# Optimization experiments

Measured on AMD Instinct MI355X. Metric: run time of the kernel, lower is better.

Reference implementation:

```python
import jax, jax.numpy as jnp
import numpy as np

N = 20000      # tuple-graph nodes
E = 320000     # edges per relation
F_IN = 5189    # 80 one-hot + 3*1703 node features
DIM = 256
N_ORIG = 183   # original texas graph nodes
C = 7


def _gcn(x, W, b, src, dst, n):
    # PyG GCNConv: add self loops, symmetric deg^-1/2 normalization, aggregate src->dst.
    loop = jnp.arange(n)
    s = jnp.concatenate([src, loop])
    d = jnp.concatenate([dst, loop])
    deg = jax.ops.segment_sum(jnp.ones(s.shape[0], x.dtype), d, num_segments=n)
    dinv = jnp.where(deg > 0, jax.lax.rsqrt(deg), 0.0)
    norm = dinv[s] * dinv[d]            # [E+n]
    h = x @ W                            # [n, dim]
    out = jax.ops.segment_sum(h[s] * norm[:, None], d, num_segments=n)
    return out + b


def _mlp(h, w1, b1, w2, b2):
    return jnp.maximum(h @ w1 + b1, 0.0) @ w2 + b2


def _seg_mean(h, idx, n):
    s = jax.ops.segment_sum(h, idx, num_segments=n)
    cnt = jax.ops.segment_sum(jnp.ones(idx.shape[0], h.dtype), idx, num_segments=n)
    return s / jnp.maximum(cnt, 1.0)[:, None]


def setup_inputs() -> dict:
    key = jax.random.key(0)
    ks = jax.random.split(key, 16)
    sc_in = 1.0 / np.sqrt(F_IN)
    sc_d = 1.0 / np.sqrt(DIM)
    sc_3d = 1.0 / np.sqrt(3 * DIM)
    inp = {
        'x': jax.random.normal(ks[0], (N, F_IN), jnp.float32),
        'w1': jax.random.normal(ks[1], (3, F_IN, DIM), jnp.float32) * sc_in,
        'b1': jnp.zeros((3, DIM), jnp.float32),
        'w2': jax.random.normal(ks[2], (3, DIM, DIM), jnp.float32) * sc_d,
        'b2': jnp.zeros((3, DIM), jnp.float32),
        'm1w1': jax.random.normal(ks[3], (3 * DIM, DIM), jnp.float32) * sc_3d,
        'm1b1': jnp.zeros((DIM,), jnp.float32),
        'm1w2': jax.random.normal(ks[4], (DIM, DIM), jnp.float32) * sc_d,
        'm1b2': jnp.zeros((DIM,), jnp.float32),
        'm2w1': jax.random.normal(ks[5], (3 * DIM, DIM), jnp.float32) * sc_3d,
        'm2b1': jnp.zeros((DIM,), jnp.float32),
        'm2w2': jax.random.normal(ks[6], (DIM, DIM), jnp.float32) * sc_d,
        'm2b2': jnp.zeros((DIM,), jnp.float32),
        'mw1': jax.random.normal(ks[7], (3 * DIM, DIM), jnp.float32) * sc_3d,
        'mb1': jnp.zeros((DIM,), jnp.float32),
        'mw2': jax.random.normal(ks[8], (DIM, C), jnp.float32) * sc_d,
        'mb2': jnp.zeros((C,), jnp.float32),
        'edge_index_1': jax.random.randint(ks[9], (2, E), 0, N),
        'edge_index_2': jax.random.randint(ks[10], (2, E), 0, N),
        'edge_index_3': jax.random.randint(ks[11], (2, E), 0, N),
        'index_1': jax.random.randint(ks[12], (N,), 0, N_ORIG),
        'index_2': jax.random.randint(ks[13], (N,), 0, N_ORIG),
        'index_3': jax.random.randint(ks[14], (N,), 0, N_ORIG),
    }
    return inp


def reference(x, w1, b1, w2, b2, m1w1, m1b1, m1w2, m1b2,
              m2w1, m2b1, m2w2, m2b2, mw1, mb1, mw2, mb2,
              edge_index_1, edge_index_2, edge_index_3,
              index_1, index_2, index_3):
    n = x.shape[0]
    eis = (edge_index_1, edge_index_2, edge_index_3)
    # layer 1: three GCN convs over the three relations, ReLU, concat, MLP
    hs = [jnp.maximum(_gcn(x, w1[i], b1[i], eis[i][0], eis[i][1], n), 0.0) for i in range(3)]
    h = _mlp(jnp.concatenate(hs, axis=-1), m1w1, m1b1, m1w2, m1b2)
    # layer 2
    hs = [jnp.maximum(_gcn(h, w2[i], b2[i], eis[i][0], eis[i][1], n), 0.0) for i in range(3)]
    h = _mlp(jnp.concatenate(hs, axis=-1), m2w1, m2b1, m2w2, m2b2)
    # faithful to source bug: index_2 is overwritten by index_3 before scatter
    x1 = _seg_mean(h, index_1, N_ORIG)
    x2 = _seg_mean(h, index_3, N_ORIG)
    x3 = _seg_mean(h, index_3, N_ORIG)
    out = _mlp(jnp.concatenate([x1, x2, x3], axis=1), mw1, mb1, mw2, mb2)
    return jax.nn.log_softmax(out, axis=1)
```

## Files before the change

kernel.cpp:

```cpp
#include <hip/hip_runtime.h>
#include <hip/hip_bf16.h>
#include <cstdint>
#include <cstddef>

typedef __bf16 bf16_t;
typedef __bf16 bf16x8 __attribute__((ext_vector_type(8)));
typedef __bf16 bf16x4 __attribute__((ext_vector_type(4)));
typedef float f32x4 __attribute__((ext_vector_type(4)));

#define NN 20000
#define NE 320000
#define FIN 5189
#define KP1 5216
#define NORIG 183

__device__ inline f32x4 ld4u(const float* p) {
  f32x4 v; __builtin_memcpy(&v, p, 16); return v;
}

__device__ inline void gload_lds16(const bf16_t* g, bf16_t* l) {
  __builtin_amdgcn_global_load_lds(
      (const __attribute__((address_space(1))) uint32_t*)g,
      (__attribute__((address_space(3))) uint32_t*)l, 16, 0, 0);
}

__device__ inline int swz(int r) { return (r ^ (r >> 2)) & 3; }

__global__ void k_cvtpad(const float* __restrict__ x, bf16_t* __restrict__ xb) {
  const int total = NN * (KP1 / 8);
  for (int idx = blockIdx.x * 256 + threadIdx.x; idx < total; idx += gridDim.x * 256) {
    int row = idx / (KP1 / 8);
    int c8  = idx - row * (KP1 / 8);
    int col = c8 * 8;
    bf16x8 v{};
    const float* xp = x + (size_t)row * FIN + col;
    if (col + 8 <= FIN) {
      f32x4 a = ld4u(xp), b = ld4u(xp + 4);
#pragma unroll
      for (int j = 0; j < 4; ++j) { v[j] = (bf16_t)a[j]; v[4 + j] = (bf16_t)b[j]; }
    } else {
#pragma unroll
      for (int j = 0; j < 8; ++j) v[j] = (col + j < FIN) ? (bf16_t)xp[j] : (bf16_t)0.f;
    }
    *(bf16x8*)&xb[(size_t)row * KP1 + col] = v;
  }
}

__global__ __launch_bounds__(512) void k_gemm_w(
    const bf16_t* __restrict__ A, const bf16_t* __restrict__ Bt,
    bf16_t* __restrict__ C, const float* __restrict__ bias,
    int M, int N, int Kp, int relu)
{
  __shared__ __align__(16) bf16_t As[2][128 * 32];
  __shared__ __align__(16) bf16_t Bs[2][256 * 32];
  const int tid = threadIdx.x, lane = tid & 63, wave = tid >> 6;
  const int m0 = blockIdx.y * 128, n0 = blockIdx.x * 256;
  const int wr = (wave >> 2) * 64, wc = (wave & 3) * 64;
  const int fm = lane & 15, fs = lane >> 4;

  const int arow = tid >> 2, asl = tid & 3;
  const int aks = asl ^ swz(arow);
  int agrow = m0 + arow; if (agrow >= M) agrow = M - 1;
  const bf16_t* asrc = A + (size_t)agrow * Kp + aks * 8;

  const int br0 = tid >> 2, br1 = 128 + br0;
  const bf16_t* bsrc0 = Bt + (size_t)(n0 + br0) * Kp + (asl ^ swz(br0)) * 8;
  const bf16_t* bsrc1 = Bt + (size_t)(n0 + br1) * Kp + (asl ^ swz(br1)) * 8;

  bf16_t* adst  = &As[0][0] + wave * 512;
  bf16_t* bdst0 = &Bs[0][0] + wave * 512;
  bf16_t* bdst1 = &Bs[0][0] + 4096 + wave * 512;

  int aoff[4], boff[4];
#pragma unroll
  for (int i = 0; i < 4; ++i) {
    int ra = wr + i * 16 + fm;
    aoff[i] = ra * 32 + (fs ^ swz(ra)) * 8;
    int rb = wc + i * 16 + fm;
    boff[i] = rb * 32 + (fs ^ swz(rb)) * 8;
  }

  f32x4 acc[4][4];
#pragma unroll
  for (int i = 0; i < 4; ++i)
#pragma unroll
    for (int j = 0; j < 4; ++j) acc[i][j] = {0.f, 0.f, 0.f, 0.f};

#define STAGEW(buf, kof) do { \
    gload_lds16(asrc + (kof),  adst  + (buf) * (128 * 32)); \
    gload_lds16(bsrc0 + (kof), bdst0 + (buf) * (256 * 32)); \
    gload_lds16(bsrc1 + (kof), bdst1 + (buf) * (256 * 32)); \
  } while (0)

  const int NT = Kp / 32;
  STAGEW(0, 0);
  __syncthreads();
  int buf = 0;
  for (int t = 0; t < NT - 1; ++t) {
    STAGEW(buf ^ 1, (t + 1) * 32);
    bf16x8 af[4], bfv[4];
#pragma unroll
    for (int i = 0; i < 4; ++i) af[i] = *(const bf16x8*)&As[buf][aoff[i]];
#pragma unroll
    for (int j = 0; j < 4; ++j) bfv[j] = *(const bf16x8*)&Bs[buf][boff[j]];
#pragma unroll
    for (int i = 0; i < 4; ++i)
#pragma unroll
      for (int j = 0; j < 4; ++j)
        acc[i][j] = __builtin_amdgcn_mfma_f32_16x16x32_bf16(af[i], bfv[j], acc[i][j], 0, 0, 0);
    __syncthreads();
    buf ^= 1;
  }
  {
    bf16x8 af[4], bfv[4];
#pragma unroll
    for (int i = 0; i < 4; ++i) af[i] = *(const bf16x8*)&As[buf][aoff[i]];
#pragma unroll
    for (int j = 0; j < 4; ++j) bfv[j] = *(const bf16x8*)&Bs[buf][boff[j]];
#pragma unroll
    for (int i = 0; i < 4; ++i)
#pragma unroll
      for (int j = 0; j < 4; ++j)
        acc[i][j] = __builtin_amdgcn_mfma_f32_16x16x32_bf16(af[i], bfv[j], acc[i][j], 0, 0, 0);
  }

  const int ccol = n0 + wc + fm;
#pragma unroll
  for (int i = 0; i < 4; ++i) {
    const int rb2 = m0 + wr + i * 16 + (lane >> 4) * 4;
#pragma unroll
    for (int r = 0; r < 4; ++r) {
      const int row = rb2 + r;
      if (row < M) {
        bf16_t* cp = C + (size_t)row * N + ccol;
#pragma unroll
        for (int j = 0; j < 4; ++j) {
          float v = acc[i][j][r];
          if (bias) v += bias[ccol + j * 16];
          if (relu) v = fmaxf(v, 0.f);
          cp[j * 16] = (bf16_t)v;
        }
      }
    }
  }
}

__global__ __launch_bounds__(256) void k_gemm_s(
    const bf16_t* __restrict__ A, const bf16_t* __restrict__ Bt,
    bf16_t* __restrict__ C, const float* __restrict__ bias,
    int M, int N, int Kp, int relu)
{
  __shared__ __align__(16) bf16_t As[2][128 * 32];
  __shared__ __align__(16) bf16_t Bs[2][128 * 32];
  const int tid = threadIdx.x, lane = tid & 63, wave = tid >> 6;
  const int m0 = blockIdx.y * 128, n0 = blockIdx.x * 128;
  const int wr = (wave >> 1) * 64, wc = (wave & 1) * 64;
  const int fm = lane & 15, fs = lane >> 4;

  const int r0 = tid >> 2, r1 = 64 + r0, sl = tid & 3;
  int ag0 = m0 + r0; if (ag0 >= M) ag0 = M - 1;
  int ag1 = m0 + r1; if (ag1 >= M) ag1 = M - 1;
  const bf16_t* asrc0 = A + (size_t)ag0 * Kp + (sl ^ swz(r0)) * 8;
  const bf16_t* asrc1 = A + (size_t)ag1 * Kp + (sl ^ swz(r1)) * 8;
  const bf16_t* bsrc0 = Bt + (size_t)(n0 + r0) * Kp + (sl ^ swz(r0)) * 8;
  const bf16_t* bsrc1 = Bt + (size_t)(n0 + r1) * Kp + (sl ^ swz(r1)) * 8;

  bf16_t* adst0 = &As[0][0] + wave * 512;
  bf16_t* adst1 = &As[0][0] + 2048 + wave * 512;
  bf16_t* bdst0 = &Bs[0][0] + wave * 512;
  bf16_t* bdst1 = &Bs[0][0] + 2048 + wave * 512;

  int aoff[4], boff[4];
#pragma unroll
  for (int i = 0; i < 4; ++i) {
    int ra = wr + i * 16 + fm;
    aoff[i] = ra * 32 + (fs ^ swz(ra)) * 8;
    int rb = wc + i * 16 + fm;
    boff[i] = rb * 32 + (fs ^ swz(rb)) * 8;
  }

  f32x4 acc[4][4];
#pragma unroll
  for (int i = 0; i < 4; ++i)
#pragma unroll
    for (int j = 0; j < 4; ++j) acc[i][j] = {0.f, 0.f, 0.f, 0.f};

#define STAGES(buf, kof) do { \
    gload_lds16(asrc0 + (kof), adst0 + (buf) * (128 * 32)); \
    gload_lds16(asrc1 + (kof), adst1 + (buf) * (128 * 32)); \
    gload_lds16(bsrc0 + (kof), bdst0 + (buf) * (128 * 32)); \
    gload_lds16(bsrc1 + (kof), bdst1 + (buf) * (128 * 32)); \
  } while (0)

  const int NT = Kp / 32;
  STAGES(0, 0);
  __syncthreads();
  int buf = 0;
  for (int t = 0; t < NT - 1; ++t) {
    STAGES(buf ^ 1, (t + 1) * 32);
    bf16x8 af[4], bfv[4];
#pragma unroll
    for (int i = 0; i < 4; ++i) af[i] = *(const bf16x8*)&As[buf][aoff[i]];
#pragma unroll
    for (int j = 0; j < 4; ++j) bfv[j] = *(const bf16x8*)&Bs[buf][boff[j]];
#pragma unroll
    for (int i = 0; i < 4; ++i)
#pragma unroll
      for (int j = 0; j < 4; ++j)
        acc[i][j] = __builtin_amdgcn_mfma_f32_16x16x32_bf16(af[i], bfv[j], acc[i][j], 0, 0, 0);
    __syncthreads();
    buf ^= 1;
  }
  {
    bf16x8 af[4], bfv[4];
#pragma unroll
    for (int i = 0; i < 4; ++i) af[i] = *(const bf16x8*)&As[buf][aoff[i]];
#pragma unroll
    for (int j = 0; j < 4; ++j) bfv[j] = *(const bf16x8*)&Bs[buf][boff[j]];
#pragma unroll
    for (int i = 0; i < 4; ++i)
#pragma unroll
      for (int j = 0; j < 4; ++j)
        acc[i][j] = __builtin_amdgcn_mfma_f32_16x16x32_bf16(af[i], bfv[j], acc[i][j], 0, 0, 0);
  }

  const int ccol = n0 + wc + fm;
#pragma unroll
  for (int i = 0; i < 4; ++i) {
    const int rb2 = m0 + wr + i * 16 + (lane >> 4) * 4;
#pragma unroll
    for (int r = 0; r < 4; ++r) {
      const int row = rb2 + r;
      if (row < M) {
        bf16_t* cp = C + (size_t)row * N + ccol;
#pragma unroll
        for (int j = 0; j < 4; ++j) {
          float v = acc[i][j][r];
          if (bias) v += bias[ccol + j * 16];
          if (relu) v = fmaxf(v, 0.f);
          cp[j * 16] = (bf16_t)v;
        }
      }
    }
  }
}

__global__ void k_transw(const float* __restrict__ src, bf16_t* __restrict__ dst,
                         int K, int Kp)
{
  __shared__ float tile[32][33];
  const int g = blockIdx.z;
  const int k0 = blockIdx.x * 32, j0 = blockIdx.y * 32;
  const int tx = threadIdx.x, ty = threadIdx.y;
  const float* sp = src + (size_t)g * K * 256;
#pragma unroll
  for (int i = 0; i < 4; ++i) {
    int k = k0 + ty + i * 8;
    tile[ty + i * 8][tx] = (k < K) ? sp[(size_t)k * 256 + j0 + tx] : 0.f;
  }
  __syncthreads();
  bf16_t* dp = dst + (size_t)g * 256 * Kp;
#pragma unroll
  for (int i = 0; i < 4; ++i) {
    int n = j0 + ty + i * 8;
    dp[(size_t)n * Kp + k0 + tx] = (bf16_t)tile[tx][ty + i * 8];
  }
}

__global__ void k_deg(const int* __restrict__ dst, int* __restrict__ cnt, int E) {
  int e = blockIdx.x * 256 + threadIdx.x;
  if (e < E) atomicAdd(&cnt[dst[e]], 1);
}

__global__ void k_dinv(const int* __restrict__ deg, float* __restrict__ dinv) {
  int v = blockIdx.x * 256 + threadIdx.x;
  if (v < 3 * NN) dinv[v] = rsqrtf((float)(deg[v] + 1));
}

#define SCAN_T 1024
#define SCAN_CH 20
__global__ __launch_bounds__(SCAN_T) void k_scan(
    const int* __restrict__ deg, int* __restrict__ rp, int* __restrict__ cur)
{
  const int r = blockIdx.x;
  const int* d = deg + r * NN;
  int* rpr = rp + r * (NN + 1);
  int* cr  = cur + r * NN;
  __shared__ int ts[SCAN_T];
  const int t = threadIdx.x;
  const int base = t * SCAN_CH;
  int local[SCAN_CH];
  int sum = 0;
#pragma unroll
  for (int i = 0; i < SCAN_CH; ++i) {
    int v = base + i;
    int x = (v < NN) ? d[v] : 0;
    local[i] = sum; sum += x;
  }
  ts[t] = sum; __syncthreads();
  for (int ofs = 1; ofs < SCAN_T; ofs <<= 1) {
    int v = ts[t];
    int w = (t >= ofs) ? ts[t - ofs] : 0;
    __syncthreads();
    ts[t] = v + w;
    __syncthreads();
  }
  int excl = (t == 0) ? 0 : ts[t - 1];
#pragma unroll
  for (int i = 0; i < SCAN_CH; ++i) {
    int v = base + i;
    if (v < NN) { int val = excl + local[i]; rpr[v] = val; cr[v] = val; }
  }
  if (t == SCAN_T - 1) rpr[NN] = ts[SCAN_T - 1];
}

__global__ void k_bucket(const int* __restrict__ src, const int* __restrict__ dst,
                         int* __restrict__ cur, int* __restrict__ col) {
  int e = blockIdx.x * 256 + threadIdx.x;
  if (e < NE) {
    int d = dst[e];
    int pos = atomicAdd(&cur[d], 1);
    col[pos] = src[e];
  }
}

__global__ __launch_bounds__(256) void k_gatherb(
    const bf16_t* __restrict__ H, bf16_t* __restrict__ Out,
    const int* __restrict__ rp, const int* __restrict__ col,
    const float* __restrict__ dinv, const float* __restrict__ bias)
{
  const int wv = threadIdx.x >> 6, lane = threadIdx.x & 63;
  const int v = blockIdx.x * 4 + wv;
  const int r = blockIdx.y;
  const int roff = r << 8;
  const int* rpr = rp + r * (NN + 1);
  const int* cr  = col + (size_t)r * NE;
  const float* dvp = dinv + r * NN;
  const float dv = dvp[v];
  const int c0 = roff + lane * 4;

  bf16x4 hs = *(const bf16x4*)&H[(size_t)v * 768 + c0];
  float a0 = (float)hs[0] * dv, a1 = (float)hs[1] * dv,
        a2 = (float)hs[2] * dv, a3 = (float)hs[3] * dv;

  int i = rpr[v];
  const int e = rpr[v + 1];
  for (; i + 2 <= e; i += 2) {
    int s0 = cr[i], s1 = cr[i + 1];
    float d0 = dvp[s0], d1 = dvp[s1];
    bf16x4 h0 = *(const bf16x4*)&H[(size_t)s0 * 768 + c0];
    bf16x4 h1 = *(const bf16x4*)&H[(size_t)s1 * 768 + c0];
    a0 += (float)h0[0] * d0 + (float)h1[0] * d1;
    a1 += (float)h0[1] * d0 + (float)h1[1] * d1;
    a2 += (float)h0[2] * d0 + (float)h1[2] * d1;
    a3 += (float)h0[3] * d0 + (float)h1[3] * d1;
  }
  if (i < e) {
    int s = cr[i];
    float d = dvp[s];
    bf16x4 h = *(const bf16x4*)&H[(size_t)s * 768 + c0];
    a0 += (float)h[0] * d; a1 += (float)h[1] * d;
    a2 += (float)h[2] * d; a3 += (float)h[3] * d;
  }
  f32x4 bb = ld4u(bias + c0);
  bf16x4 o;
  o[0] = (bf16_t)fmaxf(dv * a0 + bb[0], 0.f);
  o[1] = (bf16_t)fmaxf(dv * a1 + bb[1], 0.f);
  o[2] = (bf16_t)fmaxf(dv * a2 + bb[2], 0.f);
  o[3] = (bf16_t)fmaxf(dv * a3 + bb[3], 0.f);
  *(bf16x4*)&Out[(size_t)v * 768 + c0] = o;
}

__global__ void k_segscatter(const bf16_t* __restrict__ h2,
                             const int* __restrict__ i1, const int* __restrict__ i3,
                             float* __restrict__ s1, float* __restrict__ s3,
                             float* __restrict__ c1, float* __restrict__ c3) {
  int v = blockIdx.x, c = threadIdx.x;
  float val = (float)h2[(size_t)v * 256 + c];
  int g1 = i1[v], g3 = i3[v];
  atomicAdd(&s1[g1 * 256 + c], val);
  atomicAdd(&s3[g3 * 256 + c], val);
  if (c == 0) { atomicAdd(&c1[g1], 1.f); atomicAdd(&c3[g3], 1.f); }
}

__global__ __launch_bounds__(256) void k_final(
    const float* __restrict__ s1, const float* __restrict__ s3,
    const float* __restrict__ c1, const float* __restrict__ c3,
    const float* __restrict__ mw1, const float* __restrict__ mb1,
    const float* __restrict__ mw2, const float* __restrict__ mb2,
    float* __restrict__ out)
{
  __shared__ float xc[768];
  __shared__ float tt[256];
  __shared__ float lg[8];
  const int g = blockIdx.x, tid = threadIdx.x;
  float inv1 = 1.f / fmaxf(c1[g], 1.f);
  float inv3 = 1.f / fmaxf(c3[g], 1.f);
  float a3 = s3[g * 256 + tid] * inv3;
  xc[tid] = s1[g * 256 + tid] * inv1;
  xc[256 + tid] = a3;
  xc[512 + tid] = a3;
  __syncthreads();
  float acc = mb1[tid];
  for (int k = 0; k < 768; ++k) acc += xc[k] * mw1[k * 256 + tid];
  tt[tid] = fmaxf(acc, 0.f);
  __syncthreads();
  if (tid < 7) {
    float a = mb2[tid];
    for (int k = 0; k < 256; ++k) a += tt[k] * mw2[k * 7 + tid];
    lg[tid] = a;
  }
  __syncthreads();
  if (tid == 0) {
    float mx = lg[0];
    for (int c2 = 1; c2 < 7; ++c2) mx = fmaxf(mx, lg[c2]);
    float sum = 0.f;
    for (int c2 = 0; c2 < 7; ++c2) sum += expf(lg[c2] - mx);
    float lse = logf(sum) + mx;
    for (int c2 = 0; c2 < 7; ++c2) out[g * 7 + c2] = lg[c2] - lse;
  }
}

extern "C" void kernel_launch(void* const* d_in, const int* in_sizes, int n_in,
                              void* d_out, int out_size, void* d_ws, size_t ws_size,
                              hipStream_t stream) {
  const float* x    = (const float*)d_in[0];
  const float* w1   = (const float*)d_in[1];
  const float* b1   = (const float*)d_in[2];
  const float* w2   = (const float*)d_in[3];
  const float* b2   = (const float*)d_in[4];
  const float* m1w1 = (const float*)d_in[5];
  const float* m1b1 = (const float*)d_in[6];
  const float* m1w2 = (const float*)d_in[7];
  const float* m1b2 = (const float*)d_in[8];
  const float* m2w1 = (const float*)d_in[9];
  const float* m2b1 = (const float*)d_in[10];
  const float* m2w2 = (const float*)d_in[11];
  const float* m2b2 = (const float*)d_in[12];
  const float* mw1  = (const float*)d_in[13];
  const float* mb1  = (const float*)d_in[14];
  const float* mw2  = (const float*)d_in[15];
  const float* mb2  = (const float*)d_in[16];
  const int* e1 = (const int*)d_in[17];
  const int* e2 = (const int*)d_in[18];
  const int* e3 = (const int*)d_in[19];
  const int* i1 = (const int*)d_in[20];
  const int* i3 = (const int*)d_in[22];
  float* out = (float*)d_out;

  char* ws = (char*)d_ws;
  size_t off = 0;
  auto alloc = [&](size_t bytes) {
    char* p = ws + off;
    off += (bytes + 255) & ~(size_t)255;
    return (void*)p;
  };
  bf16_t* xb   = (bf16_t*)alloc((size_t)NN * KP1 * 2);
  bf16_t* wt   = (bf16_t*)alloc((size_t)768 * KP1 * 2);
  bf16_t* a1   = (bf16_t*)alloc((size_t)NN * 768 * 2);
  bf16_t* g1   = (bf16_t*)alloc((size_t)NN * 768 * 2);
  bf16_t* t1   = (bf16_t*)alloc((size_t)NN * 256 * 2);
  bf16_t* h1   = (bf16_t*)alloc((size_t)NN * 256 * 2);
  int*    deg  = (int*)alloc((size_t)3 * NN * 4);
  float*  dinv = (float*)alloc((size_t)3 * NN * 4);
  int*    rp   = (int*)alloc((size_t)3 * (NN + 1) * 4);
  int*    cur  = (int*)alloc((size_t)3 * NN * 4);
  int*    col  = (int*)alloc((size_t)3 * NE * 4);
  float*  s1   = (float*)alloc((size_t)NORIG * 256 * 4);
  float*  s3   = (float*)alloc((size_t)NORIG * 256 * 4);
  float*  c1   = (float*)alloc((size_t)NORIG * 4);
  float*  c3   = (float*)alloc((size_t)NORIG * 4);

  hipMemsetAsync(deg, 0, (size_t)3 * NN * 4, stream);
  int gb = (NE + 255) / 256;
  k_deg<<<gb, 256, 0, stream>>>(e1 + NE, deg + 0 * NN, NE);
  k_deg<<<gb, 256, 0, stream>>>(e2 + NE, deg + 1 * NN, NE);
  k_deg<<<gb, 256, 0, stream>>>(e3 + NE, deg + 2 * NN, NE);
  k_dinv<<<(3 * NN + 255) / 256, 256, 0, stream>>>(deg, dinv);
  k_scan<<<3, SCAN_T, 0, stream>>>(deg, rp, cur);
  k_bucket<<<gb, 256, 0, stream>>>(e1, e1 + NE, cur + 0 * NN, col + 0 * (size_t)NE);
  k_bucket<<<gb, 256, 0, stream>>>(e2, e2 + NE, cur + 1 * NN, col + 1 * (size_t)NE);
  k_bucket<<<gb, 256, 0, stream>>>(e3, e3 + NE, cur + 2 * NN, col + 2 * (size_t)NE);

  auto transw = [&](const float* Wsrc, int G, int K, int Kp) {
    k_transw<<<dim3(Kp / 32, 8, G), dim3(32, 8), 0, stream>>>(Wsrc, wt, K, Kp);
  };

  dim3 ggat(NN / 4, 3);

  transw(w1, 3, FIN, KP1);
  k_cvtpad<<<2048, 256, 0, stream>>>(x, xb);
  k_gemm_w<<<dim3(3, 157), 512, 0, stream>>>(xb, wt, a1, nullptr, NN, 768, KP1, 0);
  k_gatherb<<<ggat, 256, 0, stream>>>(a1, g1, rp, col, dinv, b1);
  transw(m1w1, 1, 768, 768);
  k_gemm_s<<<dim3(2, 157), 256, 0, stream>>>(g1, wt, t1, m1b1, NN, 256, 768, 1);
  transw(m1w2, 1, 256, 256);
  k_gemm_s<<<dim3(2, 157), 256, 0, stream>>>(t1, wt, h1, m1b2, NN, 256, 256, 0);

  transw(w2, 3, 256, 256);
  k_gemm_w<<<dim3(3, 157), 512, 0, stream>>>(h1, wt, a1, nullptr, NN, 768, 256, 0);
  k_gatherb<<<ggat, 256, 0, stream>>>(a1, g1, rp, col, dinv, b2);
  transw(m2w1, 1, 768, 768);
  k_gemm_s<<<dim3(2, 157), 256, 0, stream>>>(g1, wt, t1, m2b1, NN, 256, 768, 1);
  transw(m2w2, 1, 256, 256);
  k_gemm_s<<<dim3(2, 157), 256, 0, stream>>>(t1, wt, h1, m2b2, NN, 256, 256, 0);

  hipMemsetAsync(s1, 0, (size_t)NORIG * 256 * 4, stream);
  hipMemsetAsync(s3, 0, (size_t)NORIG * 256 * 4, stream);
  hipMemsetAsync(c1, 0, (size_t)NORIG * 4, stream);
  hipMemsetAsync(c3, 0, (size_t)NORIG * 4, stream);
  k_segscatter<<<NN, 256, 0, stream>>>(h1, i1, i3, s1, s3, c1, c3);
  k_final<<<NORIG, 256, 0, stream>>>(s1, s3, c1, c3, mw1, mb1, mw2, mb2, out);
}
```

Measured before the change: 898.9 us.

## Enlarge wide GEMM tile to 256x256 with 4-stage global-to-LDS pipeline

Replaces the 128x256 double-buffered wide GEMM with a 256x256 tile per block, each wave computing 128x64, and a four-buffer ring that prefetches three K-steps ahead using explicit vmcnt waits and raw barriers. It also raises MFMA priority during the compute section. The aim is more operand reuse per LDS load and hiding of global-load latency in the large feature GEMM. The cost is 128 KB of LDS and many more accumulator registers, which limit occupancy, and a grid of 237 blocks that may underfill the CUs.

```diff
diff --git a/kernel.cpp b/kernel.cpp
--- a/kernel.cpp
+++ b/kernel.cpp
@@ -46,87 +46,93 @@
   }
 }
 
-__global__ __launch_bounds__(512) void k_gemm_w(
+__global__ __launch_bounds__(512, 2) void k_gemm8(
     const bf16_t* __restrict__ A, const bf16_t* __restrict__ Bt,
     bf16_t* __restrict__ C, const float* __restrict__ bias,
     int M, int N, int Kp, int relu)
 {
-  __shared__ __align__(16) bf16_t As[2][128 * 32];
-  __shared__ __align__(16) bf16_t Bs[2][256 * 32];
+  __shared__ __align__(16) bf16_t As[4][256 * 32];
+  __shared__ __align__(16) bf16_t Bs[4][256 * 32];
   const int tid = threadIdx.x, lane = tid & 63, wave = tid >> 6;
-  const int m0 = blockIdx.y * 128, n0 = blockIdx.x * 256;
-  const int wr = (wave >> 2) * 64, wc = (wave & 3) * 64;
+  const int m0 = blockIdx.y * 256, n0 = blockIdx.x * 256;
+  const int wr = (wave >> 2) * 128, wc = (wave & 3) * 64;
   const int fm = lane & 15, fs = lane >> 4;
 
-  const int arow = tid >> 2, asl = tid & 3;
-  const int aks = asl ^ swz(arow);
-  int agrow = m0 + arow; if (agrow >= M) agrow = M - 1;
-  const bf16_t* asrc = A + (size_t)agrow * Kp + aks * 8;
-
-  const int br0 = tid >> 2, br1 = 128 + br0;
-  const bf16_t* bsrc0 = Bt + (size_t)(n0 + br0) * Kp + (asl ^ swz(br0)) * 8;
-  const bf16_t* bsrc1 = Bt + (size_t)(n0 + br1) * Kp + (asl ^ swz(br1)) * 8;
-
-  bf16_t* adst  = &As[0][0] + wave * 512;
-  bf16_t* bdst0 = &Bs[0][0] + wave * 512;
-  bf16_t* bdst1 = &Bs[0][0] + 4096 + wave * 512;
-
-  int aoff[4], boff[4];
-#pragma unroll
-  for (int i = 0; i < 4; ++i) {
+  const int rA0 = 32 * wave + (lane >> 2);
+  const int rA1 = rA0 + 16;
+  const int p0 = lane & 3;
+  int gmA0 = m0 + rA0; if (gmA0 >= M) gmA0 = M - 1;
+  int gmA1 = m0 + rA1; if (gmA1 >= M) gmA1 = M - 1;
+  const bf16_t* srcA0 = A + (size_t)gmA0 * Kp + (p0 ^ swz(rA0)) * 8;
+  const bf16_t* srcA1 = A + (size_t)gmA1 * Kp + (p0 ^ swz(rA1)) * 8;
+  const bf16_t* srcB0 = Bt + (size_t)(n0 + rA0) * Kp + (p0 ^ swz(rA0)) * 8;
+  const bf16_t* srcB1 = Bt + (size_t)(n0 + rA1) * Kp + (p0 ^ swz(rA1)) * 8;
+  const int dst0 = 1024 * wave;
+  const int dst1 = 1024 * wave + 512;
+
+  int aoff[8], boff[4];
+#pragma unroll
+  for (int i = 0; i < 8; ++i) {
     int ra = wr + i * 16 + fm;
     aoff[i] = ra * 32 + (fs ^ swz(ra)) * 8;
-    int rb = wc + i * 16 + fm;
-    boff[i] = rb * 32 + (fs ^ swz(rb)) * 8;
-  }
-
-  f32x4 acc[4][4];
-#pragma unroll
-  for (int i = 0; i < 4; ++i)
+  }
+#pragma unroll
+  for (int j = 0; j < 4; ++j) {
+    int rb = wc + j * 16 + fm;
+    boff[j] = rb * 32 + (fs ^ swz(rb)) * 8;
+  }
+
+  f32x4 acc[8][4];
+#pragma unroll
+  for (int i = 0; i < 8; ++i)
 #pragma unroll
     for (int j = 0; j < 4; ++j) acc[i][j] = {0.f, 0.f, 0.f, 0.f};
 
-#define STAGEW(buf, kof) do { \
-    gload_lds16(asrc + (kof),  adst  + (buf) * (128 * 32)); \
-    gload_lds16(bsrc0 + (kof), bdst0 + (buf) * (256 * 32)); \
-    gload_lds16(bsrc1 + (kof), bdst1 + (buf) * (256 * 32)); \
+#define STG8(s) do { \
+    const int b_ = (s) & 3; const int ko_ = (s) * 32; \
+    gload_lds16(srcA0 + ko_, &As[b_][0] + dst0); \
+    gload_lds16(srcA1 + ko_, &As[b_][0] + dst1); \
+    gload_lds16(srcB0 + ko_, &Bs[b_][0] + dst0); \
+    gload_lds16(srcB1 + ko_, &Bs[b_][0] + dst1); \
   } while (0)
 
   const int NT = Kp / 32;
-  STAGEW(0, 0);
-  __syncthreads();
-  int buf = 0;
-  for (int t = 0; t < NT - 1; ++t) {
-    STAGEW(buf ^ 1, (t + 1) * 32);
-    bf16x8 af[4], bfv[4];
-#pragma unroll
-    for (int i = 0; i < 4; ++i) af[i] = *(const bf16x8*)&As[buf][aoff[i]];
-#pragma unroll
-    for (int j = 0; j < 4; ++j) bfv[j] = *(const bf16x8*)&Bs[buf][boff[j]];
-#pragma unroll
-    for (int i = 0; i < 4; ++i)
+  STG8(0); STG8(1); STG8(2);
+  __builtin_amdgcn_sched_barrier(0);
+  asm volatile("s_waitcnt vmcnt(8)" ::: "memory");
+  __builtin_amdgcn_s_barrier();
+  __builtin_amdgcn_sched_barrier(0);
+
+  for (int t = 0; t < NT; ++t) {
+    const int nxt = t + 3;
+    if (nxt < NT) STG8(nxt);
+    const int b = t & 3;
+    bf16x8 af[8], bfv[4];
+#pragma unroll
+    for (int j = 0; j < 4; ++j) bfv[j] = *(const bf16x8*)&Bs[b][boff[j]];
+#pragma unroll
+    for (int i = 0; i < 8; ++i) af[i] = *(const bf16x8*)&As[b][aoff[i]];
+    __builtin_amdgcn_s_setprio(1);
+#pragma unroll
+    for (int i = 0; i < 8; ++i)
 #pragma unroll
       for (int j = 0; j < 4; ++j)
         acc[i][j] = __builtin_amdgcn_mfma_f32_16x16x32_bf16(af[i], bfv[j], acc[i][j], 0, 0, 0);
-    __syncthreads();
-    buf ^= 1;
-  }
-  {
-    bf16x8 af[4], bfv[4];
-#pragma unroll
-    for (int i = 0; i < 4; ++i) af[i] = *(const bf16x8*)&As[buf][aoff[i]];
-#pragma unroll
-    for (int j = 0; j < 4; ++j) bfv[j] = *(const bf16x8*)&Bs[buf][boff[j]];
-#pragma unroll
-    for (int i = 0; i < 4; ++i)
-#pragma unroll
-      for (int j = 0; j < 4; ++j)
-        acc[i][j] = __builtin_amdgcn_mfma_f32_16x16x32_bf16(af[i], bfv[j], acc[i][j], 0, 0, 0);
-  }
+    __builtin_amdgcn_s_setprio(0);
+    if (t < NT - 1) {
+      __builtin_amdgcn_sched_barrier(0);
+      if (nxt < NT)            asm volatile("s_waitcnt vmcnt(8) lgkmcnt(0)" ::: "memory");
+      else if (nxt == NT)      asm volatile("s_waitcnt vmcnt(4) lgkmcnt(0)" ::: "memory");
+      else                     asm volatile("s_waitcnt vmcnt(0) lgkmcnt(0)" ::: "memory");
+      __builtin_amdgcn_s_barrier();
+      __builtin_amdgcn_sched_barrier(0);
+    }
+  }
+#undef STG8
 
   const int ccol = n0 + wc + fm;
 #pragma unroll
-  for (int i = 0; i < 4; ++i) {
+  for (int i = 0; i < 8; ++i) {
     const int rb2 = m0 + wr + i * 16 + (lane >> 4) * 4;
 #pragma unroll
     for (int r = 0; r < 4; ++r) {
@@ -490,7 +496,7 @@
 
   transw(w1, 3, FIN, KP1);
   k_cvtpad<<<2048, 256, 0, stream>>>(x, xb);
-  k_gemm_w<<<dim3(3, 157), 512, 0, stream>>>(xb, wt, a1, nullptr, NN, 768, KP1, 0);
+  k_gemm8<<<dim3(3, 79), 512, 0, stream>>>(xb, wt, a1, nullptr, NN, 768, KP1, 0);
   k_gatherb<<<ggat, 256, 0, stream>>>(a1, g1, rp, col, dinv, b1);
   transw(m1w1, 1, 768, 768);
   k_gemm_s<<<dim3(2, 157), 256, 0, stream>>>(g1, wt, t1, m1b1, NN, 256, 768, 1);
@@ -498,7 +504,7 @@
   k_gemm_s<<<dim3(2, 157), 256, 0, stream>>>(t1, wt, h1, m1b2, NN, 256, 256, 0);
 
   transw(w2, 3, 256, 256);
-  k_gemm_w<<<dim3(3, 157), 512, 0, stream>>>(h1, wt, a1, nullptr, NN, 768, 256, 0);
+  k_gemm8<<<dim3(3, 79), 512, 0, stream>>>(h1, wt, a1, nullptr, NN, 768, 256, 0);
   k_gatherb<<<ggat, 256, 0, stream>>>(a1, g1, rp, col, dinv, b2);
   transw(m2w1, 1, 768, 768);
   k_gemm_s<<<dim3(2, 157), 256, 0, stream>>>(g1, wt, t1, m2b1, NN, 256, 768, 1);
```

Result: slower. 961.3 us (+6.9%).

## Replace atomic segment-mean with CSR gather, merge degree/bucket kernels, XCD-remap GEMM

Applied to the files above, without the earlier changes.

The float-atomic scatter used for the final segment means is replaced by a CSR build over the 183 groups (count, scan, bucket) and a gather-based reduction inside the final MLP kernel. The per-relation degree and bucket kernels are merged into single launches. The wide GEMM now uses a 1D grid with a chiplet-aware (XCD) block remap for better L2 locality, and the edge-gather loop is unrolled by four. This removes about 10M float atomics and several launches and memsets, but the final kernel now serially reads about 110 rows per group per thread.

```diff
diff --git a/kernel.cpp b/kernel.cpp
--- a/kernel.cpp
+++ b/kernel.cpp
@@ -49,12 +49,18 @@
 __global__ __launch_bounds__(512) void k_gemm_w(
     const bf16_t* __restrict__ A, const bf16_t* __restrict__ Bt,
     bf16_t* __restrict__ C, const float* __restrict__ bias,
-    int M, int N, int Kp, int relu)
+    int M, int N, int Kp, int relu, int NBX)
 {
   __shared__ __align__(16) bf16_t As[2][128 * 32];
   __shared__ __align__(16) bf16_t Bs[2][256 * 32];
+  const int nwg = gridDim.x;
+  const int q = nwg >> 3, rr = nwg & 7;
+  const int xcd = blockIdx.x & 7, jj = blockIdx.x >> 3;
+  const int L = (xcd < rr ? xcd * (q + 1) : rr * (q + 1) + (xcd - rr) * q) + jj;
+  const int bx = L % NBX, by = L / NBX;
+
   const int tid = threadIdx.x, lane = tid & 63, wave = tid >> 6;
-  const int m0 = blockIdx.y * 128, n0 = blockIdx.x * 256;
+  const int m0 = by * 128, n0 = bx * 256;
   const int wr = (wave >> 2) * 64, wc = (wave & 3) * 64;
   const int fm = lane & 15, fs = lane >> 4;
 
@@ -267,9 +273,22 @@
   }
 }
 
-__global__ void k_deg(const int* __restrict__ dst, int* __restrict__ cnt, int E) {
-  int e = blockIdx.x * 256 + threadIdx.x;
-  if (e < E) atomicAdd(&cnt[dst[e]], 1);
+__global__ void k_deg3(const int* __restrict__ e1, const int* __restrict__ e2,
+                       const int* __restrict__ e3, int* __restrict__ deg) {
+  int i = blockIdx.x * 256 + threadIdx.x;
+  if (i >= 3 * NE) return;
+  int r = i / NE, e = i - r * NE;
+  const int* d = (r == 0 ? e1 : (r == 1 ? e2 : e3)) + NE;
+  atomicAdd(&deg[r * NN + d[e]], 1);
+}
+
+__global__ void k_degi(const int* __restrict__ i1, const int* __restrict__ i3,
+                       int* __restrict__ deg183) {
+  int i = blockIdx.x * 256 + threadIdx.x;
+  if (i >= 2 * NN) return;
+  int r = i / NN, v = i - r * NN;
+  int g = (r ? i3 : i1)[v];
+  atomicAdd(&deg183[r * NORIG + g], 1);
 }
 
 __global__ void k_dinv(const int* __restrict__ deg, float* __restrict__ dinv) {
@@ -314,14 +333,50 @@
   if (t == SCAN_T - 1) rpr[NN] = ts[SCAN_T - 1];
 }
 
-__global__ void k_bucket(const int* __restrict__ src, const int* __restrict__ dst,
-                         int* __restrict__ cur, int* __restrict__ col) {
-  int e = blockIdx.x * 256 + threadIdx.x;
-  if (e < NE) {
-    int d = dst[e];
-    int pos = atomicAdd(&cur[d], 1);
-    col[pos] = src[e];
-  }
+__global__ void k_scan183(const int* __restrict__ deg183, int* __restrict__ rpg,
+                          int* __restrict__ cur183) {
+  const int r = blockIdx.x;
+  const int* d = deg183 + r * NORIG;
+  int* rpr = rpg + r * (NORIG + 1);
+  int* cr  = cur183 + r * NORIG;
+  __shared__ int ts[256];
+  const int t = threadIdx.x;
+  int x = (t < NORIG) ? d[t] : 0;
+  ts[t] = x; __syncthreads();
+  for (int o = 1; o < 256; o <<= 1) {
+    int v = ts[t];
+    int w = (t >= o) ? ts[t - o] : 0;
+    __syncthreads();
+    ts[t] = v + w;
+    __syncthreads();
+  }
+  if (t < NORIG) {
+    int excl = ts[t] - x;
+    rpr[t] = excl; cr[t] = excl;
+    if (t == NORIG - 1) rpr[NORIG] = ts[t];
+  }
+}
+
+__global__ void k_bucket3(const int* __restrict__ e1, const int* __restrict__ e2,
+                          const int* __restrict__ e3, int* __restrict__ cur,
+                          int* __restrict__ col) {
+  int i = blockIdx.x * 256 + threadIdx.x;
+  if (i >= 3 * NE) return;
+  int r = i / NE, e = i - r * NE;
+  const int* ei = (r == 0 ? e1 : (r == 1 ? e2 : e3));
+  int d = ei[NE + e];
+  int pos = atomicAdd(&cur[r * NN + d], 1);
+  col[(size_t)r * NE + pos] = ei[e];
+}
+
+__global__ void k_bucketi(const int* __restrict__ i1, const int* __restrict__ i3,
+                          int* __restrict__ cur183, int* __restrict__ colg) {
+  int i = blockIdx.x * 256 + threadIdx.x;
+  if (i >= 2 * NN) return;
+  int r = i / NN, v = i - r * NN;
+  int g = (r ? i3 : i1)[v];
+  int pos = atomicAdd(&cur183[r * NORIG + g], 1);
+  colg[r * NN + pos] = v;
 }
 
 __global__ __launch_bounds__(256) void k_gatherb(
@@ -345,17 +400,19 @@
 
   int i = rpr[v];
   const int e = rpr[v + 1];
-  for (; i + 2 <= e; i += 2) {
-    int s0 = cr[i], s1 = cr[i + 1];
-    float d0 = dvp[s0], d1 = dvp[s1];
+  for (; i + 4 <= e; i += 4) {
+    int s0 = cr[i], s1 = cr[i + 1], s2 = cr[i + 2], s3 = cr[i + 3];
+    float d0 = dvp[s0], d1 = dvp[s1], d2 = dvp[s2], d3 = dvp[s3];
     bf16x4 h0 = *(const bf16x4*)&H[(size_t)s0 * 768 + c0];
     bf16x4 h1 = *(const bf16x4*)&H[(size_t)s1 * 768 + c0];
-    a0 += (float)h0[0] * d0 + (float)h1[0] * d1;
-    a1 += (float)h0[1] * d0 + (float)h1[1] * d1;
-    a2 += (float)h0[2] * d0 + (float)h1[2] * d1;
-    a3 += (float)h0[3] * d0 + (float)h1[3] * d1;
-  }
-  if (i < e) {
+    bf16x4 h2 = *(const bf16x4*)&H[(size_t)s2 * 768 + c0];
+    bf16x4 h3 = *(const bf16x4*)&H[(size_t)s3 * 768 + c0];
+    a0 += (float)h0[0] * d0 + (float)h1[0] * d1 + (float)h2[0] * d2 + (float)h3[0] * d3;
+    a1 += (float)h0[1] * d0 + (float)h1[1] * d1 + (float)h2[1] * d2 + (float)h3[1] * d3;
+    a2 += (float)h0[2] * d0 + (float)h1[2] * d1 + (float)h2[2] * d2 + (float)h3[2] * d3;
+    a3 += (float)h0[3] * d0 + (float)h1[3] * d1 + (float)h2[3] * d2 + (float)h3[3] * d3;
+  }
+  for (; i < e; ++i) {
     int s = cr[i];
     float d = dvp[s];
     bf16x4 h = *(const bf16x4*)&H[(size_t)s * 768 + c0];
@@ -371,21 +428,9 @@
   *(bf16x4*)&Out[(size_t)v * 768 + c0] = o;
 }
 
-__global__ void k_segscatter(const bf16_t* __restrict__ h2,
-                             const int* __restrict__ i1, const int* __restrict__ i3,
-                             float* __restrict__ s1, float* __restrict__ s3,
-                             float* __restrict__ c1, float* __restrict__ c3) {
-  int v = blockIdx.x, c = threadIdx.x;
-  float val = (float)h2[(size_t)v * 256 + c];
-  int g1 = i1[v], g3 = i3[v];
-  atomicAdd(&s1[g1 * 256 + c], val);
-  atomicAdd(&s3[g3 * 256 + c], val);
-  if (c == 0) { atomicAdd(&c1[g1], 1.f); atomicAdd(&c3[g3], 1.f); }
-}
-
-__global__ __launch_bounds__(256) void k_final(
-    const float* __restrict__ s1, const float* __restrict__ s3,
-    const float* __restrict__ c1, const float* __restrict__ c3,
+__global__ __launch_bounds__(256) void k_final2(
+    const bf16_t* __restrict__ h2,
+    const int* __restrict__ rpg, const int* __restrict__ colg,
     const float* __restrict__ mw1, const float* __restrict__ mb1,
     const float* __restrict__ mw2, const float* __restrict__ mb2,
     float* __restrict__ out)
@@ -394,10 +439,20 @@
   __shared__ float tt[256];
   __shared__ float lg[8];
   const int g = blockIdx.x, tid = threadIdx.x;
-  float inv1 = 1.f / fmaxf(c1[g], 1.f);
-  float inv3 = 1.f / fmaxf(c3[g], 1.f);
-  float a3 = s3[g * 256 + tid] * inv3;
-  xc[tid] = s1[g * 256 + tid] * inv1;
+  const int* rp1 = rpg;
+  const int* rp3 = rpg + (NORIG + 1);
+  const int* c1v = colg;
+  const int* c3v = colg + NN;
+
+  float a1 = 0.f;
+  int b1 = rp1[g], e1 = rp1[g + 1];
+  for (int i = b1; i < e1; ++i) a1 += (float)h2[(size_t)c1v[i] * 256 + tid];
+  float a3 = 0.f;
+  int b3 = rp3[g], e3 = rp3[g + 1];
+  for (int i = b3; i < e3; ++i) a3 += (float)h2[(size_t)c3v[i] * 256 + tid];
+  a1 *= 1.f / fmaxf((float)(e1 - b1), 1.f);
+  a3 *= 1.f / fmaxf((float)(e3 - b3), 1.f);
+  xc[tid] = a1;
   xc[256 + tid] = a3;
   xc[512 + tid] = a3;
   __syncthreads();
@@ -461,36 +516,35 @@
   bf16_t* g1   = (bf16_t*)alloc((size_t)NN * 768 * 2);
   bf16_t* t1   = (bf16_t*)alloc((size_t)NN * 256 * 2);
   bf16_t* h1   = (bf16_t*)alloc((size_t)NN * 256 * 2);
-  int*    deg  = (int*)alloc((size_t)3 * NN * 4);
+  int*    deg  = (int*)alloc(((size_t)3 * NN + 2 * NORIG) * 4);
   float*  dinv = (float*)alloc((size_t)3 * NN * 4);
   int*    rp   = (int*)alloc((size_t)3 * (NN + 1) * 4);
   int*    cur  = (int*)alloc((size_t)3 * NN * 4);
   int*    col  = (int*)alloc((size_t)3 * NE * 4);
-  float*  s1   = (float*)alloc((size_t)NORIG * 256 * 4);
-  float*  s3   = (float*)alloc((size_t)NORIG * 256 * 4);
-  float*  c1   = (float*)alloc((size_t)NORIG * 4);
-  float*  c3   = (float*)alloc((size_t)NORIG * 4);
-
-  hipMemsetAsync(deg, 0, (size_t)3 * NN * 4, stream);
-  int gb = (NE + 255) / 256;
-  k_deg<<<gb, 256, 0, stream>>>(e1 + NE, deg + 0 * NN, NE);
-  k_deg<<<gb, 256, 0, stream>>>(e2 + NE, deg + 1 * NN, NE);
-  k_deg<<<gb, 256, 0, stream>>>(e3 + NE, deg + 2 * NN, NE);
+  int*    rpg  = (int*)alloc((size_t)2 * (NORIG + 1) * 4);
+  int*    cur183 = (int*)alloc((size_t)2 * NORIG * 4);
+  int*    colg = (int*)alloc((size_t)2 * NN * 4);
+  int*    deg183 = deg + 3 * NN;
+
+  hipMemsetAsync(deg, 0, ((size_t)3 * NN + 2 * NORIG) * 4, stream);
+  k_deg3<<<(3 * NE + 255) / 256, 256, 0, stream>>>(e1, e2, e3, deg);
+  k_degi<<<(2 * NN + 255) / 256, 256, 0, stream>>>(i1, i3, deg183);
   k_dinv<<<(3 * NN + 255) / 256, 256, 0, stream>>>(deg, dinv);
   k_scan<<<3, SCAN_T, 0, stream>>>(deg, rp, cur);
-  k_bucket<<<gb, 256, 0, stream>>>(e1, e1 + NE, cur + 0 * NN, col + 0 * (size_t)NE);
-  k_bucket<<<gb, 256, 0, stream>>>(e2, e2 + NE, cur + 1 * NN, col + 1 * (size_t)NE);
-  k_bucket<<<gb, 256, 0, stream>>>(e3, e3 + NE, cur + 2 * NN, col + 2 * (size_t)NE);
+  k_scan183<<<2, 256, 0, stream>>>(deg183, rpg, cur183);
+  k_bucket3<<<(3 * NE + 255) / 256, 256, 0, stream>>>(e1, e2, e3, cur, col);
+  k_bucketi<<<(2 * NN + 255) / 256, 256, 0, stream>>>(i1, i3, cur183, colg);
 
   auto transw = [&](const float* Wsrc, int G, int K, int Kp) {
     k_transw<<<dim3(Kp / 32, 8, G), dim3(32, 8), 0, stream>>>(Wsrc, wt, K, Kp);
   };
 
   dim3 ggat(NN / 4, 3);
+  const int NWG = 3 * 157;
 
   transw(w1, 3, FIN, KP1);
   k_cvtpad<<<2048, 256, 0, stream>>>(x, xb);
-  k_gemm_w<<<dim3(3, 157), 512, 0, stream>>>(xb, wt, a1, nullptr, NN, 768, KP1, 0);
+  k_gemm_w<<<NWG, 512, 0, stream>>>(xb, wt, a1, nullptr, NN, 768, KP1, 0, 3);
   k_gatherb<<<ggat, 256, 0, stream>>>(a1, g1, rp, col, dinv, b1);
   transw(m1w1, 1, 768, 768);
   k_gemm_s<<<dim3(2, 157), 256, 0, stream>>>(g1, wt, t1, m1b1, NN, 256, 768, 1);
@@ -498,17 +552,12 @@
   k_gemm_s<<<dim3(2, 157), 256, 0, stream>>>(t1, wt, h1, m1b2, NN, 256, 256, 0);
 
   transw(w2, 3, 256, 256);
-  k_gemm_w<<<dim3(3, 157), 512, 0, stream>>>(h1, wt, a1, nullptr, NN, 768, 256, 0);
+  k_gemm_w<<<NWG, 512, 0, stream>>>(h1, wt, a1, nullptr, NN, 768, 256, 0, 3);
   k_gatherb<<<ggat, 256, 0, stream>>>(a1, g1, rp, col, dinv, b2);
   transw(m2w1, 1, 768, 768);
   k_gemm_s<<<dim3(2, 157), 256, 0, stream>>>(g1, wt, t1, m2b1, NN, 256, 768, 1);
   transw(m2w2, 1, 256, 256);
   k_gemm_s<<<dim3(2, 157), 256, 0, stream>>>(t1, wt, h1, m2b2, NN, 256, 256, 0);
 
-  hipMemsetAsync(s1, 0, (size_t)NORIG * 256 * 4, stream);
-  hipMemsetAsync(s3, 0, (size_t)NORIG * 256 * 4, stream);
-  hipMemsetAsync(c1, 0, (size_t)NORIG * 4, stream);
-  hipMemsetAsync(c3, 0, (size_t)NORIG * 4, stream);
-  k_segscatter<<<NN, 256, 0, stream>>>(h1, i1, i3, s1, s3, c1, c3);
-  k_final<<<NORIG, 256, 0, stream>>>(s1, s3, c1, c3, mw1, mb1, mw2, mb2, out);
-}
+  k_final2<<<NORIG, 256, 0, stream>>>(h1, rpg, colg, mw1, mb1, mw2, mb2, out);
+}
```

New measurement: 872.0 us. 1.03x faster.
